# Performance work log

Measured on AMD Instinct MI355X. Metric: run time of the kernel, lower is better.

## Reference

```python
import jax, jax.numpy as jnp
import numpy as np

N_NODES = 100000
N_EDGES = 1600000
D_IN, D_HID, D_OUT = 128, 64, 64


def setup_inputs() -> dict:
    key = jax.random.key(0)
    k0, k1, k2, k3 = jax.random.split(key, 4)
    X = jax.random.normal(k0, (N_NODES, D_IN), dtype=jnp.float32)
    E = jax.random.randint(k1, (2, N_EDGES), 0, N_NODES, dtype=jnp.int32)
    W1 = jax.random.normal(k2, (D_IN, D_HID), dtype=jnp.float32) * 0.05
    b1 = jnp.zeros((D_HID,), dtype=jnp.float32)
    W2 = jax.random.normal(k3, (D_HID, D_OUT), dtype=jnp.float32) * 0.05
    b2 = jnp.zeros((D_OUT,), dtype=jnp.float32)
    return {"V": N_NODES, "E": E, "X": X, "W1": W1, "b1": b1, "W2": W2, "b2": b2}


def _gcn_layer(X, W, b, src, dst, norm, n):
    # GCNConv: linear transform (no bias), gather, degree-normalize, scatter-add, + bias
    Xl = X @ W                              # [n, d_out]
    msg = Xl[src] * norm[:, None]           # [n_edges_sl, d_out] gather
    out = jax.ops.segment_sum(msg, dst, num_segments=n)  # scatter-add
    return out + b


def reference(V, E, X, W1, b1, W2, b2):
    n = X.shape[0]
    # add self loops (add_self_loops=True)
    loop = jnp.arange(n, dtype=E.dtype)
    src = jnp.concatenate([E[0], loop])
    dst = jnp.concatenate([E[1], loop])
    # symmetric gcn_norm: deg over target nodes (unit edge weights)
    deg = jax.ops.segment_sum(jnp.ones_like(dst, dtype=X.dtype), dst, num_segments=n)
    dinv = jnp.where(deg > 0, jax.lax.rsqrt(deg), 0.0)
    norm = dinv[src] * dinv[dst]
    H = jax.nn.relu(_gcn_layer(X, W1, b1, src, dst, norm, n))
    # last layer: no ReLU (matches torch module)
    return _gcn_layer(H, W2, b2, src, dst, norm, n)
```

## Files before the change

### kernel.cpp

```cpp
#include <hip/hip_runtime.h>

#define NT 256
#define NG 512
#define NB 1024
#define TILE 256
#define TILE_SH 8
#define BSTRIDE 8192
#define BSTRIDE_SH 13
#define EPB 4096
#define ITB 16
#define NBUCK_PAD 512

static inline int cdiv(long long a, long long b) { return (int)((a + b - 1) / b); }

typedef unsigned int uint32;
typedef unsigned short ushort16;
typedef short bf16x8 __attribute__((ext_vector_type(8)));
typedef float f32x4 __attribute__((ext_vector_type(4)));

__device__ __forceinline__ ushort16 f2bf(float f) {
  uint32 u = __float_as_uint(f);
  u = (u + 0x7FFF + ((u >> 16) & 1)) >> 16;
  return (ushort16)u;
}
__device__ __forceinline__ float bflo(uint32 w) { return __uint_as_float(w << 16); }
__device__ __forceinline__ float bfhi(uint32 w) { return __uint_as_float(w & 0xFFFF0000u); }
__device__ __forceinline__ float bf2f(ushort16 h) { return __uint_as_float(((uint32)h) << 16); }

template <int K, int NTH>
__device__ __forceinline__ void stage_W(const float* __restrict__ W,
                                        unsigned short* __restrict__ Wt) {
  constexpr int STR = K + 8;
  for (int i = threadIdx.x; i < K * 64; i += NTH) {
    int k = i >> 6, nn = i & 63;
    Wt[nn * STR + k] = f2bf(W[i]);
  }
}

template <int K, int SPLIT>
__device__ __forceinline__ void gemm_tile(const void* __restrict__ Xp,
                                          const unsigned short* __restrict__ Wt,
                                          uint2* __restrict__ Yb, int n, int base) {
  constexpr int STR = K + 8;
  const int tid = threadIdx.x;
  const int w = tid >> 6;
  const int lane = tid & 63;
  const int r = lane & 15;
  const int quad = lane >> 4;
  const int rloc = w * 16 + r;
  const int v = base + rloc;

  f32x4 acc[4];
#pragma unroll
  for (int i = 0; i < 4; ++i) acc[i] = (f32x4)(0.f);

  const float4* X4 = (const float4*)Xp;
  float4 a[K / 32][2];
#pragma unroll
  for (int ks = 0; ks < K / 32; ++ks) {
    a[ks][0] = make_float4(0.f, 0.f, 0.f, 0.f);
    a[ks][1] = make_float4(0.f, 0.f, 0.f, 0.f);
    if (v < n) {
      a[ks][0] = X4[(size_t)v * (K / 4) + ks * 8 + quad * 2];
      a[ks][1] = X4[(size_t)v * (K / 4) + ks * 8 + quad * 2 + 1];
    }
  }
#pragma unroll
  for (int ks = 0; ks < K / 32; ++ks) {
    float f[8] = {a[ks][0].x, a[ks][0].y, a[ks][0].z, a[ks][0].w,
                  a[ks][1].x, a[ks][1].y, a[ks][1].z, a[ks][1].w};
    bf16x8 xh, xl;
#pragma unroll
    for (int j = 0; j < 8; ++j) {
      ushort16 h = f2bf(f[j]);
      xh[j] = (short)h;
      if (SPLIT) xl[j] = (short)f2bf(f[j] - bf2f(h));
    }
    const int koff = ks * 32 + quad * 8;
#pragma unroll
    for (int nt = 0; nt < 4; ++nt) {
      bf16x8 wf = *(const bf16x8*)&Wt[(nt * 16 + r) * STR + koff];
      if (SPLIT)
        acc[nt] = __builtin_amdgcn_mfma_f32_16x16x32_bf16(wf, xl, acc[nt], 0, 0, 0);
      acc[nt] = __builtin_amdgcn_mfma_f32_16x16x32_bf16(wf, xh, acc[nt], 0, 0, 0);
    }
  }

  if (v < n) {
#pragma unroll
    for (int nt = 0; nt < 4; ++nt) {
      uint2 u;
      u.x = (uint32)f2bf(acc[nt][0]) | ((uint32)f2bf(acc[nt][1]) << 16);
      u.y = (uint32)f2bf(acc[nt][2]) | ((uint32)f2bf(acc[nt][3]) << 16);
      Yb[(size_t)v * 16 + nt * 4 + quad] = u;
    }
  }
}

template <int K>
__device__ __forceinline__ void gemm_tile_lds8(const unsigned short* __restrict__ Hs,
                                               const unsigned short* __restrict__ Wt,
                                               uint2* __restrict__ Yb, int n,
                                               int base) {
  constexpr int STR = K + 8;
  const int tid = threadIdx.x;
  const int w = tid >> 6;
  const int wr = w & 3;
  const int nh = w >> 2;
  const int lane = tid & 63;
  const int r = lane & 15;
  const int quad = lane >> 4;
  const int rloc = wr * 16 + r;
  const int v = base + rloc;

  f32x4 acc[2];
#pragma unroll
  for (int i = 0; i < 2; ++i) acc[i] = (f32x4)(0.f);
#pragma unroll
  for (int ks = 0; ks < K / 32; ++ks) {
    const int koff = ks * 32 + quad * 8;
    bf16x8 xf = *(const bf16x8*)&Hs[rloc * STR + koff];
#pragma unroll
    for (int i = 0; i < 2; ++i) {
      const int nt = nh * 2 + i;
      bf16x8 wf = *(const bf16x8*)&Wt[(nt * 16 + r) * STR + koff];
      acc[i] = __builtin_amdgcn_mfma_f32_16x16x32_bf16(wf, xf, acc[i], 0, 0, 0);
    }
  }
  if (v < n) {
#pragma unroll
    for (int i = 0; i < 2; ++i) {
      const int nt = nh * 2 + i;
      uint2 u;
      u.x = (uint32)f2bf(acc[i][0]) | ((uint32)f2bf(acc[i][1]) << 16);
      u.y = (uint32)f2bf(acc[i][2]) | ((uint32)f2bf(acc[i][3]) << 16);
      Yb[(size_t)v * 16 + nt * 4 + quad] = u;
    }
  }
}

struct ScatSh {
  int cnt[NBUCK_PAD];
  int lcur[NBUCK_PAD];
  int delta[NBUCK_PAD];
  int hs[NT];
  uint32 sorted[EPB];
  unsigned short bid[EPB];
};
union FusedSh {
  unsigned short wt[64 * 136];
  ScatSh s;
};

__global__ __launch_bounds__(NT, 4) void k_fused(
    const int* __restrict__ src, const int* __restrict__ dst,
    int* __restrict__ bcursor, int* __restrict__ tileCtr,
    uint32* __restrict__ buck, int nE, int nbuck, int gscat, int ntile,
    const float* __restrict__ X, const float* __restrict__ W1,
    uint2* __restrict__ Yb, int n) {
  __shared__ FusedSh sm;
  __shared__ int stile;
  const int t = threadIdx.x;
  if ((int)blockIdx.x < gscat) {
    for (int i = t; i < NBUCK_PAD; i += NT) sm.s.cnt[i] = 0;
    __syncthreads();
    const int e0 = blockIdx.x * EPB;
    const int ne = min(EPB, nE - e0);
    int dreg[ITB];
#pragma unroll
    for (int it = 0; it < ITB; ++it) {
      int e = e0 + it * NT + t;
      dreg[it] = (e < nE) ? dst[e] : -1;
      if (dreg[it] >= 0) atomicAdd(&sm.s.cnt[dreg[it] >> TILE_SH], 1);
    }
    __syncthreads();
    int c0 = sm.s.cnt[2 * t], c1 = sm.s.cnt[2 * t + 1];
    int ps = c0 + c1;
    sm.s.hs[t] = ps;
    __syncthreads();
    for (int o = 1; o < NT; o <<= 1) {
      int x = (t >= o) ? sm.s.hs[t - o] : 0;
      __syncthreads();
      sm.s.hs[t] += x;
      __syncthreads();
    }
    int lb0 = sm.s.hs[t] - ps;
    int lb1 = lb0 + c0;
    sm.s.lcur[2 * t] = lb0;
    sm.s.lcur[2 * t + 1] = lb1;
    {
      int b0 = 2 * t, b1 = 2 * t + 1;
      if (b0 < nbuck) {
        int g0 = c0 ? atomicAdd(&bcursor[b0], c0) : 0;
        sm.s.delta[b0] = (b0 << BSTRIDE_SH) + g0 - lb0;
      }
      if (b1 < nbuck) {
        int g1 = c1 ? atomicAdd(&bcursor[b1], c1) : 0;
        sm.s.delta[b1] = (b1 << BSTRIDE_SH) + g1 - lb1;
      }
    }
    __syncthreads();
#pragma unroll
    for (int it = 0; it < ITB; ++it) {
      int e = e0 + it * NT + t;
      if (dreg[it] >= 0) {
        int d = dreg[it];
        int b = d >> TILE_SH;
        int p = atomicAdd(&sm.s.lcur[b], 1);
        sm.s.sorted[p] = (uint32)src[e] | ((uint32)(d & (TILE - 1)) << 24);
        sm.s.bid[p] = (unsigned short)b;
      }
    }
    __syncthreads();
    for (int i = t; i < ne; i += NT) {
      int b = sm.s.bid[i];
      int g = sm.s.delta[b] + i;
      if (g < ((b + 1) << BSTRIDE_SH))
        buck[g] = sm.s.sorted[i];
    }
    __syncthreads();
  }
  stage_W<128, NT>(W1, sm.wt);
  __syncthreads();
  for (;;) {
    if (t == 0) stile = atomicAdd(tileCtr, 1);
    __syncthreads();
    int tile = stile;
    __syncthreads();
    if (tile >= ntile) break;
    gemm_tile<128, 1>(X, sm.wt, Yb, n, tile * 64);
  }
}

__global__ __launch_bounds__(NB) void k_bcsr(const uint32* __restrict__ buck,
                                             const int* __restrict__ bcursor,
                                             int2* __restrict__ rowspan,
                                             float* __restrict__ dinv,
                                             int* __restrict__ srcs, int n) {
  __shared__ int hist[TILE];
  __shared__ int hs[TILE];
  __shared__ int off[TILE];
  __shared__ uint32 sarr[BSTRIDE];
  const int b = blockIdx.x;
  const int t = threadIdx.x;
  const int W = b * BSTRIDE;
  const int cntb = min(bcursor[b], BSTRIDE);
  const int v0 = b << TILE_SH;
  const int nv = min(TILE, n - v0);
  if (t < TILE) hist[t] = 0;
  __syncthreads();
  for (int i = t; i < cntb; i += NB) atomicAdd(&hist[buck[W + i] >> 24], 1);
  __syncthreads();
  int h = (t < TILE) ? hist[t] : 0;
  if (t < TILE) hs[t] = h;
  __syncthreads();
  for (int o = 1; o < TILE; o <<= 1) {
    int x = (t >= o && t < TILE) ? hs[t - o] : 0;
    __syncthreads();
    if (t < TILE) hs[t] += x;
    __syncthreads();
  }
  if (t < TILE) {
    int ex = hs[t] - h;
    off[t] = ex;
    if (t < nv) {
      rowspan[v0 + t] = make_int2(W + ex, W + ex + h);
      dinv[v0 + t] = rsqrtf((float)(h + 1));
    }
  }
  __syncthreads();
  for (int i = t; i < cntb; i += NB) {
    uint32 w = buck[W + i];
    int ld = (int)(w >> 24);
    int p = atomicAdd(&off[ld], 1);
    sarr[p] = w & 0x00FFFFFFu;
  }
  __syncthreads();
  for (int i = t; i < cntb; i += NB) srcs[W + i] = (int)sarr[i];
}

struct Acc8 {
  float a0, a1, a2, a3, a4, a5, a6, a7;
  __device__ __forceinline__ void madd(uint4 r, float s) {
    a0 = fmaf(bflo(r.x), s, a0); a1 = fmaf(bfhi(r.x), s, a1);
    a2 = fmaf(bflo(r.y), s, a2); a3 = fmaf(bfhi(r.y), s, a3);
    a4 = fmaf(bflo(r.z), s, a4); a5 = fmaf(bfhi(r.z), s, a5);
    a6 = fmaf(bflo(r.w), s, a6); a7 = fmaf(bfhi(r.w), s, a7);
  }
};

__device__ __forceinline__ void agg_node(const int* __restrict__ srcs,
                                         const float* __restrict__ dinv,
                                         const uint4* __restrict__ Y, int beg,
                                         int end, int part, int q, Acc8& A) {
  int j = beg + q;
  for (; j + 12 < end; j += 16) {
    int s0 = srcs[j];
    int s1 = srcs[j + 4];
    int s2 = srcs[j + 8];
    int s3 = srcs[j + 12];
    float d0 = dinv[s0], d1 = dinv[s1], d2 = dinv[s2], d3 = dinv[s3];
    uint4 r0 = Y[(size_t)s0 * 8 + part];
    uint4 r1 = Y[(size_t)s1 * 8 + part];
    uint4 r2 = Y[(size_t)s2 * 8 + part];
    uint4 r3 = Y[(size_t)s3 * 8 + part];
    A.madd(r0, d0);
    A.madd(r1, d1);
    A.madd(r2, d2);
    A.madd(r3, d3);
  }
  if (j + 4 < end) {
    int s0 = srcs[j];
    int s1 = srcs[j + 4];
    float d0 = dinv[s0], d1 = dinv[s1];
    uint4 r0 = Y[(size_t)s0 * 8 + part];
    uint4 r1 = Y[(size_t)s1 * 8 + part];
    A.madd(r0, d0);
    A.madd(r1, d1);
    j += 8;
  }
  if (j < end) {
    int s = srcs[j];
    A.madd(Y[(size_t)s * 8 + part], dinv[s]);
  }
}

#define L1STR 72

__global__ __launch_bounds__(NG, 4) void k_gather_l1(
    const int2* __restrict__ rowspan, const int* __restrict__ srcs,
    const float* __restrict__ dinv, const uint4* __restrict__ Y1,
    const float* __restrict__ bias, const float* __restrict__ W2,
    uint2* __restrict__ Y2, int n) {
  __shared__ unsigned short Wt[64 * L1STR];
  __shared__ unsigned short Hs[64 * L1STR];
  stage_W<64, NG>(W2, Wt);

  const int tid = threadIdx.x;
  const int lane = tid & 63;
  const int l5 = lane & 31;
  const int part = l5 & 7;
  const int q = l5 >> 3;
  const int grp = ((tid >> 6) << 1) + (lane >> 5);
  const int base = blockIdx.x * 64;

#pragma unroll 1
  for (int p = 0; p < 4; ++p) {
    const int local = p * 16 + grp;
    const int v = base + local;
    const bool act = v < n;
    int2 rs = act ? rowspan[v] : make_int2(0, 0);
    const float dv = act ? dinv[v] : 0.f;
    uint4 wv = act ? Y1[(size_t)v * 8 + part] : make_uint4(0u, 0u, 0u, 0u);
    Acc8 A = {0.f, 0.f, 0.f, 0.f, 0.f, 0.f, 0.f, 0.f};
    agg_node(srcs, dinv, Y1, rs.x, rs.y, part, q, A);
#pragma unroll
    for (int m = 8; m <= 16; m <<= 1) {
      A.a0 += __shfl_xor(A.a0, m);
      A.a1 += __shfl_xor(A.a1, m);
      A.a2 += __shfl_xor(A.a2, m);
      A.a3 += __shfl_xor(A.a3, m);
      A.a4 += __shfl_xor(A.a4, m);
      A.a5 += __shfl_xor(A.a5, m);
      A.a6 += __shfl_xor(A.a6, m);
      A.a7 += __shfl_xor(A.a7, m);
    }
    if (q == 0 && act) {
      const float4* b4 = (const float4*)bias;
      float4 b0 = b4[part * 2], b1 = b4[part * 2 + 1];
      float r0 = fmaxf(dv * (A.a0 + dv * bflo(wv.x)) + b0.x, 0.f);
      float r1 = fmaxf(dv * (A.a1 + dv * bfhi(wv.x)) + b0.y, 0.f);
      float r2 = fmaxf(dv * (A.a2 + dv * bflo(wv.y)) + b0.z, 0.f);
      float r3 = fmaxf(dv * (A.a3 + dv * bfhi(wv.y)) + b0.w, 0.f);
      float r4 = fmaxf(dv * (A.a4 + dv * bflo(wv.z)) + b1.x, 0.f);
      float r5 = fmaxf(dv * (A.a5 + dv * bfhi(wv.z)) + b1.y, 0.f);
      float r6 = fmaxf(dv * (A.a6 + dv * bflo(wv.w)) + b1.z, 0.f);
      float r7 = fmaxf(dv * (A.a7 + dv * bfhi(wv.w)) + b1.w, 0.f);
      uint4 u;
      u.x = (uint32)f2bf(r0) | ((uint32)f2bf(r1) << 16);
      u.y = (uint32)f2bf(r2) | ((uint32)f2bf(r3) << 16);
      u.z = (uint32)f2bf(r4) | ((uint32)f2bf(r5) << 16);
      u.w = (uint32)f2bf(r6) | ((uint32)f2bf(r7) << 16);
      *(uint4*)&Hs[local * L1STR + part * 8] = u;
    }
  }
  __syncthreads();
  gemm_tile_lds8<64>(Hs, Wt, Y2, n, base);
}

__global__ __launch_bounds__(NT) void k_gather2(const int2* __restrict__ rowspan,
                                                const int* __restrict__ srcs,
                                                const float* __restrict__ dinv,
                                                const uint4* __restrict__ Xn,
                                                const float* __restrict__ bias,
                                                float* __restrict__ outp, int n) {
  const int gt = blockIdx.x * NT + threadIdx.x;
  const int lane = threadIdx.x & 63;
  const int v = ((gt >> 6) << 1) + (lane >> 5);
  if (v >= n) return;
  const int l5 = lane & 31;
  const int part = l5 & 7;
  const int q = l5 >> 3;
  const int2 rs = rowspan[v];
  const float dv = dinv[v];
  uint4 wv = Xn[(size_t)v * 8 + part];
  Acc8 A = {0.f, 0.f, 0.f, 0.f, 0.f, 0.f, 0.f, 0.f};
  agg_node(srcs, dinv, Xn, rs.x, rs.y, part, q, A);
#pragma unroll
  for (int m = 8; m <= 16; m <<= 1) {
    A.a0 += __shfl_xor(A.a0, m);
    A.a1 += __shfl_xor(A.a1, m);
    A.a2 += __shfl_xor(A.a2, m);
    A.a3 += __shfl_xor(A.a3, m);
    A.a4 += __shfl_xor(A.a4, m);
    A.a5 += __shfl_xor(A.a5, m);
    A.a6 += __shfl_xor(A.a6, m);
    A.a7 += __shfl_xor(A.a7, m);
  }
  if (q == 0) {
    const float4* b4 = (const float4*)bias;
    float4 b0 = b4[part * 2], b1 = b4[part * 2 + 1];
    float r0 = dv * (A.a0 + dv * bflo(wv.x)) + b0.x;
    float r1 = dv * (A.a1 + dv * bfhi(wv.x)) + b0.y;
    float r2 = dv * (A.a2 + dv * bflo(wv.y)) + b0.z;
    float r3 = dv * (A.a3 + dv * bfhi(wv.y)) + b0.w;
    float r4 = dv * (A.a4 + dv * bflo(wv.z)) + b1.x;
    float r5 = dv * (A.a5 + dv * bfhi(wv.z)) + b1.y;
    float r6 = dv * (A.a6 + dv * bflo(wv.w)) + b1.z;
    float r7 = dv * (A.a7 + dv * bfhi(wv.w)) + b1.w;
    float4* o4 = (float4*)outp;
    o4[(size_t)v * 16 + part * 2] = make_float4(r0, r1, r2, r3);
    o4[(size_t)v * 16 + part * 2 + 1] = make_float4(r4, r5, r6, r7);
  }
}

extern "C" void kernel_launch(void* const* d_in, const int* in_sizes, int n_in,
                              void* d_out, int out_size, void* d_ws, size_t ws_size,
                              hipStream_t stream) {
  const int* E = (const int*)d_in[1];
  const float* X = (const float*)d_in[2];
  const float* W1 = (const float*)d_in[3];
  const float* b1 = (const float*)d_in[4];
  const float* W2 = (const float*)d_in[5];
  const float* b2 = (const float*)d_in[6];
  float* out = (float*)d_out;

  const int n = in_sizes[2] / 128;
  const int nE = in_sizes[1] / 2;
  const int* src = E;
  const int* dst = E + nE;
  const int nbuck = cdiv(n, TILE);

  char* ws = (char*)d_ws;
  size_t off = 0;
  auto alloc = [&](size_t bytes) {
    size_t o = off;
    off = (off + bytes + 255) & ~(size_t)255;
    return (void*)(ws + o);
  };
  int2* rowspan = (int2*)alloc((size_t)n * 8);
  float* dinv = (float*)alloc((size_t)n * 4);
  int* bcursor = (int*)alloc((size_t)(nbuck + 1) * 4);
  int* tileCtr = bcursor + nbuck;
  uint32* buck = (uint32*)alloc((size_t)nbuck * BSTRIDE * 4);
  int* srcs = (int*)alloc((size_t)nbuck * BSTRIDE * 4);
  uint2* Y1 = (uint2*)alloc((size_t)n * 64 * 2);
  uint2* Y2 = (uint2*)alloc((size_t)n * 64 * 2);

  const int gscat = cdiv(nE, EPB);
  const int ntile = cdiv(n, 64);
  const int gfused = 1024;
  const int gthreads_blocks = cdiv((long long)n * 32, NT);

  hipMemsetAsync(bcursor, 0, (size_t)(nbuck + 1) * 4, stream);

  k_fused<<<gfused, NT, 0, stream>>>(src, dst, bcursor, tileCtr, buck, nE,
                                     nbuck, gscat, ntile, X, W1, Y1, n);
  k_bcsr<<<nbuck, NB, 0, stream>>>(buck, bcursor, rowspan, dinv, srcs, n);

  k_gather_l1<<<ntile, NG, 0, stream>>>(rowspan, srcs, dinv, (const uint4*)Y1,
                                        b1, W2, Y2, n);

  k_gather2<<<gthreads_blocks, NT, 0, stream>>>(rowspan, srcs, dinv,
                                                (const uint4*)Y2, b2, out, n);
}
```

Before: 239.7 us.

## Split layer-1 GEMM tiles between scatter and bucket-CSR kernels for overlap

Splits the dense X@W1 tile work into two parts. The first SPLIT tiles run in the scatter-fused kernel and the rest run in the bucket-CSR kernel, which now also stages W1 and pulls tiles from a second counter after building CSR rows. Tiles are claimed four at a time to reduce atomic traffic. The scatter chunk size is halved and grid and occupancy bounds are raised so more blocks share the scatter phase. The intent is to hide the latency-bound sort phases behind GEMM work, at the cost of a fixed split constant tuned for this graph size and a larger grid in the second kernel.

```diff
diff --git a/kernel.cpp b/kernel.cpp
--- a/kernel.cpp
+++ b/kernel.cpp
@@ -7,9 +7,10 @@
 #define TILE_SH 8
 #define BSTRIDE 8192
 #define BSTRIDE_SH 13
-#define EPB 4096
-#define ITB 16
+#define EPB 2048
+#define ITB 8
 #define NBUCK_PAD 512
+#define SPLIT 768
 
 static inline int cdiv(long long a, long long b) { return (int)((a + b - 1) / b); }
 
@@ -37,12 +38,12 @@
   }
 }
 
-template <int K, int SPLIT>
+template <int K, int SPLITLO>
 __device__ __forceinline__ void gemm_tile(const void* __restrict__ Xp,
                                           const unsigned short* __restrict__ Wt,
-                                          uint2* __restrict__ Yb, int n, int base) {
+                                          uint2* __restrict__ Yb, int n, int base,
+                                          int tid) {
   constexpr int STR = K + 8;
-  const int tid = threadIdx.x;
   const int w = tid >> 6;
   const int lane = tid & 63;
   const int r = lane & 15;
@@ -74,13 +75,13 @@
     for (int j = 0; j < 8; ++j) {
       ushort16 h = f2bf(f[j]);
       xh[j] = (short)h;
-      if (SPLIT) xl[j] = (short)f2bf(f[j] - bf2f(h));
+      if (SPLITLO) xl[j] = (short)f2bf(f[j] - bf2f(h));
     }
     const int koff = ks * 32 + quad * 8;
 #pragma unroll
     for (int nt = 0; nt < 4; ++nt) {
       bf16x8 wf = *(const bf16x8*)&Wt[(nt * 16 + r) * STR + koff];
-      if (SPLIT)
+      if (SPLITLO)
         acc[nt] = __builtin_amdgcn_mfma_f32_16x16x32_bf16(wf, xl, acc[nt], 0, 0, 0);
       acc[nt] = __builtin_amdgcn_mfma_f32_16x16x32_bf16(wf, xh, acc[nt], 0, 0, 0);
     }
@@ -152,10 +153,10 @@
   ScatSh s;
 };
 
-__global__ __launch_bounds__(NT, 4) void k_fused(
+__global__ __launch_bounds__(NT, 6) void k_fused(
     const int* __restrict__ src, const int* __restrict__ dst,
     int* __restrict__ bcursor, int* __restrict__ tileCtr,
-    uint32* __restrict__ buck, int nE, int nbuck, int gscat, int ntile,
+    uint32* __restrict__ buck, int nE, int nbuck, int gscat, int split,
     const float* __restrict__ X, const float* __restrict__ W1,
     uint2* __restrict__ Yb, int n) {
   __shared__ FusedSh sm;
@@ -223,60 +224,89 @@
   stage_W<128, NT>(W1, sm.wt);
   __syncthreads();
   for (;;) {
-    if (t == 0) stile = atomicAdd(tileCtr, 1);
-    __syncthreads();
-    int tile = stile;
-    __syncthreads();
-    if (tile >= ntile) break;
-    gemm_tile<128, 1>(X, sm.wt, Yb, n, tile * 64);
-  }
-}
-
-__global__ __launch_bounds__(NB) void k_bcsr(const uint32* __restrict__ buck,
-                                             const int* __restrict__ bcursor,
-                                             int2* __restrict__ rowspan,
-                                             float* __restrict__ dinv,
-                                             int* __restrict__ srcs, int n) {
-  __shared__ int hist[TILE];
-  __shared__ int hs[TILE];
-  __shared__ int off[TILE];
-  __shared__ uint32 sarr[BSTRIDE];
+    if (t == 0) stile = atomicAdd(tileCtr, 4);
+    __syncthreads();
+    const int base = stile;
+    __syncthreads();
+    if (base >= split) break;
+#pragma unroll 1
+    for (int c = 0; c < 4; ++c) {
+      int tile = base + c;
+      if (tile < split) gemm_tile<128, 1>(X, sm.wt, Yb, n, tile * 64, t);
+    }
+  }
+}
+
+union BcsrSh {
+  struct {
+    int hist[TILE];
+    int hs[TILE];
+    int off[TILE];
+    uint32 sarr[BSTRIDE];
+  } c;
+  unsigned short wt[64 * 136];
+};
+
+__global__ __launch_bounds__(NB, 8) void k_bcsr_gemm(
+    const uint32* __restrict__ buck, const int* __restrict__ bcursor,
+    int2* __restrict__ rowspan, float* __restrict__ dinv,
+    int* __restrict__ srcs, int n, int nbuck, const float* __restrict__ X,
+    const float* __restrict__ W1, uint2* __restrict__ Yb,
+    int* __restrict__ tileCtr2, int split, int ntile) {
+  __shared__ BcsrSh sm;
+  __shared__ int stile;
+  const int t = threadIdx.x;
   const int b = blockIdx.x;
-  const int t = threadIdx.x;
-  const int W = b * BSTRIDE;
-  const int cntb = min(bcursor[b], BSTRIDE);
-  const int v0 = b << TILE_SH;
-  const int nv = min(TILE, n - v0);
-  if (t < TILE) hist[t] = 0;
+  if (b < nbuck) {
+    const int W = b * BSTRIDE;
+    const int cntb = min(bcursor[b], BSTRIDE);
+    const int v0 = b << TILE_SH;
+    const int nv = min(TILE, n - v0);
+    if (t < TILE) sm.c.hist[t] = 0;
+    __syncthreads();
+    for (int i = t; i < cntb; i += NB) atomicAdd(&sm.c.hist[buck[W + i] >> 24], 1);
+    __syncthreads();
+    int h = (t < TILE) ? sm.c.hist[t] : 0;
+    if (t < TILE) sm.c.hs[t] = h;
+    __syncthreads();
+    for (int o = 1; o < TILE; o <<= 1) {
+      int x = (t >= o && t < TILE) ? sm.c.hs[t - o] : 0;
+      __syncthreads();
+      if (t < TILE) sm.c.hs[t] += x;
+      __syncthreads();
+    }
+    if (t < TILE) {
+      int ex = sm.c.hs[t] - h;
+      sm.c.off[t] = ex;
+      if (t < nv) {
+        rowspan[v0 + t] = make_int2(W + ex, W + ex + h);
+        dinv[v0 + t] = rsqrtf((float)(h + 1));
+      }
+    }
+    __syncthreads();
+    for (int i = t; i < cntb; i += NB) {
+      uint32 w = buck[W + i];
+      int ld = (int)(w >> 24);
+      int p = atomicAdd(&sm.c.off[ld], 1);
+      sm.c.sarr[p] = w & 0x00FFFFFFu;
+    }
+    __syncthreads();
+    for (int i = t; i < cntb; i += NB) srcs[W + i] = (int)sm.c.sarr[i];
+    __syncthreads();
+  }
+  stage_W<128, NB>(W1, sm.wt);
   __syncthreads();
-  for (int i = t; i < cntb; i += NB) atomicAdd(&hist[buck[W + i] >> 24], 1);
-  __syncthreads();
-  int h = (t < TILE) ? hist[t] : 0;
-  if (t < TILE) hs[t] = h;
-  __syncthreads();
-  for (int o = 1; o < TILE; o <<= 1) {
-    int x = (t >= o && t < TILE) ? hs[t - o] : 0;
-    __syncthreads();
-    if (t < TILE) hs[t] += x;
-    __syncthreads();
-  }
-  if (t < TILE) {
-    int ex = hs[t] - h;
-    off[t] = ex;
-    if (t < nv) {
-      rowspan[v0 + t] = make_int2(W + ex, W + ex + h);
-      dinv[v0 + t] = rsqrtf((float)(h + 1));
-    }
-  }
-  __syncthreads();
-  for (int i = t; i < cntb; i += NB) {
-    uint32 w = buck[W + i];
-    int ld = (int)(w >> 24);
-    int p = atomicAdd(&off[ld], 1);
-    sarr[p] = w & 0x00FFFFFFu;
-  }
-  __syncthreads();
-  for (int i = t; i < cntb; i += NB) srcs[W + i] = (int)sarr[i];
+  const int g = t >> 8;
+  const int lt = t & 255;
+  for (;;) {
+    if (t == 0) stile = atomicAdd(tileCtr2, 4);
+    __syncthreads();
+    const int base = split + stile;
+    __syncthreads();
+    if (base >= ntile) break;
+    const int tile = base + g;
+    if (tile < ntile) gemm_tile<128, 1>(X, sm.wt, Yb, n, tile * 64, lt);
+  }
 }
 
 struct Acc8 {
@@ -460,8 +490,9 @@
   };
   int2* rowspan = (int2*)alloc((size_t)n * 8);
   float* dinv = (float*)alloc((size_t)n * 4);
-  int* bcursor = (int*)alloc((size_t)(nbuck + 1) * 4);
+  int* bcursor = (int*)alloc((size_t)(nbuck + 2) * 4);
   int* tileCtr = bcursor + nbuck;
+  int* tileCtr2 = bcursor + nbuck + 1;
   uint32* buck = (uint32*)alloc((size_t)nbuck * BSTRIDE * 4);
   int* srcs = (int*)alloc((size_t)nbuck * BSTRIDE * 4);
   uint2* Y1 = (uint2*)alloc((size_t)n * 64 * 2);
@@ -469,14 +500,15 @@
 
   const int gscat = cdiv(nE, EPB);
   const int ntile = cdiv(n, 64);
-  const int gfused = 1024;
+  const int gfused = 1536;
   const int gthreads_blocks = cdiv((long long)n * 32, NT);
 
-  hipMemsetAsync(bcursor, 0, (size_t)(nbuck + 1) * 4, stream);
+  hipMemsetAsync(bcursor, 0, (size_t)(nbuck + 2) * 4, stream);
 
   k_fused<<<gfused, NT, 0, stream>>>(src, dst, bcursor, tileCtr, buck, nE,
-                                     nbuck, gscat, ntile, X, W1, Y1, n);
-  k_bcsr<<<nbuck, NB, 0, stream>>>(buck, bcursor, rowspan, dinv, srcs, n);
+                                     nbuck, gscat, SPLIT, X, W1, Y1, n);
+  k_bcsr_gemm<<<1024, NB, 0, stream>>>(buck, bcursor, rowspan, dinv, srcs, n,
+                                       nbuck, X, W1, Y1, tileCtr2, SPLIT, ntile);
 
   k_gather_l1<<<ntile, NG, 0, stream>>>(rowspan, srcs, dinv, (const uint4*)Y1,
                                         b1, W2, Y2, n);
```

After: 257.7 us. 1.07x slower.

## Use 512-thread fused blocks with static GEMM tile split instead of atomic tile counter

Applied to the files above, without the earlier changes.

Doubles the fused scatter/GEMM kernel block size to 512 threads, which halves per-thread edge iterations and turns the bucket scan into one bucket per thread. The dynamic atomic tile counter is replaced by a static assignment: non-scatter blocks take the first T0 tiles and scatter blocks take the rest in a strided loop, with tiles now covering 128 rows across 8 waves. This removes the per-tile global atomic and its two barriers. The static split may unbalance work, because scatter blocks start their GEMM tiles late, and occupancy changes with the larger blocks.

```diff
diff --git a/kernel.cpp b/kernel.cpp
--- a/kernel.cpp
+++ b/kernel.cpp
@@ -1,6 +1,7 @@
 #include <hip/hip_runtime.h>
 
 #define NT 256
+#define NF 512
 #define NG 512
 #define NB 1024
 #define TILE 256
@@ -8,8 +9,9 @@
 #define BSTRIDE 8192
 #define BSTRIDE_SH 13
 #define EPB 4096
-#define ITB 16
+#define ITB 8
 #define NBUCK_PAD 512
+#define GTILE 128
 
 static inline int cdiv(long long a, long long b) { return (int)((a + b - 1) / b); }
 
@@ -37,18 +39,17 @@
   }
 }
 
-template <int K, int SPLIT>
-__device__ __forceinline__ void gemm_tile(const void* __restrict__ Xp,
-                                          const unsigned short* __restrict__ Wt,
-                                          uint2* __restrict__ Yb, int n, int base) {
+template <int K>
+__device__ __forceinline__ void gemm_tile8(const float* __restrict__ Xp,
+                                           const unsigned short* __restrict__ Wt,
+                                           uint2* __restrict__ Yb, int n, int base) {
   constexpr int STR = K + 8;
   const int tid = threadIdx.x;
   const int w = tid >> 6;
   const int lane = tid & 63;
   const int r = lane & 15;
   const int quad = lane >> 4;
-  const int rloc = w * 16 + r;
-  const int v = base + rloc;
+  const int v = base + w * 16 + r;
 
   f32x4 acc[4];
 #pragma unroll
@@ -74,14 +75,13 @@
     for (int j = 0; j < 8; ++j) {
       ushort16 h = f2bf(f[j]);
       xh[j] = (short)h;
-      if (SPLIT) xl[j] = (short)f2bf(f[j] - bf2f(h));
+      xl[j] = (short)f2bf(f[j] - bf2f(h));
     }
     const int koff = ks * 32 + quad * 8;
 #pragma unroll
     for (int nt = 0; nt < 4; ++nt) {
       bf16x8 wf = *(const bf16x8*)&Wt[(nt * 16 + r) * STR + koff];
-      if (SPLIT)
-        acc[nt] = __builtin_amdgcn_mfma_f32_16x16x32_bf16(wf, xl, acc[nt], 0, 0, 0);
+      acc[nt] = __builtin_amdgcn_mfma_f32_16x16x32_bf16(wf, xl, acc[nt], 0, 0, 0);
       acc[nt] = __builtin_amdgcn_mfma_f32_16x16x32_bf16(wf, xh, acc[nt], 0, 0, 0);
     }
   }
@@ -143,7 +143,7 @@
   int cnt[NBUCK_PAD];
   int lcur[NBUCK_PAD];
   int delta[NBUCK_PAD];
-  int hs[NT];
+  int hs[NF];
   uint32 sorted[EPB];
   unsigned short bid[EPB];
 };
@@ -152,57 +152,46 @@
   ScatSh s;
 };
 
-__global__ __launch_bounds__(NT, 4) void k_fused(
+__global__ __launch_bounds__(NF) void k_fused(
     const int* __restrict__ src, const int* __restrict__ dst,
-    int* __restrict__ bcursor, int* __restrict__ tileCtr,
-    uint32* __restrict__ buck, int nE, int nbuck, int gscat, int ntile,
-    const float* __restrict__ X, const float* __restrict__ W1,
-    uint2* __restrict__ Yb, int n) {
+    int* __restrict__ bcursor, uint32* __restrict__ buck, int nE, int nbuck,
+    int gscat, int t0, int ntile, const float* __restrict__ X,
+    const float* __restrict__ W1, uint2* __restrict__ Yb, int n) {
   __shared__ FusedSh sm;
-  __shared__ int stile;
   const int t = threadIdx.x;
-  if ((int)blockIdx.x < gscat) {
-    for (int i = t; i < NBUCK_PAD; i += NT) sm.s.cnt[i] = 0;
+  const bool isScat = (int)blockIdx.x < gscat;
+  if (isScat) {
+    sm.s.cnt[t] = 0;
     __syncthreads();
     const int e0 = blockIdx.x * EPB;
     const int ne = min(EPB, nE - e0);
     int dreg[ITB];
 #pragma unroll
     for (int it = 0; it < ITB; ++it) {
-      int e = e0 + it * NT + t;
+      int e = e0 + it * NF + t;
       dreg[it] = (e < nE) ? dst[e] : -1;
       if (dreg[it] >= 0) atomicAdd(&sm.s.cnt[dreg[it] >> TILE_SH], 1);
     }
     __syncthreads();
-    int c0 = sm.s.cnt[2 * t], c1 = sm.s.cnt[2 * t + 1];
-    int ps = c0 + c1;
-    sm.s.hs[t] = ps;
-    __syncthreads();
-    for (int o = 1; o < NT; o <<= 1) {
+    int c = sm.s.cnt[t];
+    sm.s.hs[t] = c;
+    __syncthreads();
+    for (int o = 1; o < NF; o <<= 1) {
       int x = (t >= o) ? sm.s.hs[t - o] : 0;
       __syncthreads();
       sm.s.hs[t] += x;
       __syncthreads();
     }
-    int lb0 = sm.s.hs[t] - ps;
-    int lb1 = lb0 + c0;
-    sm.s.lcur[2 * t] = lb0;
-    sm.s.lcur[2 * t + 1] = lb1;
-    {
-      int b0 = 2 * t, b1 = 2 * t + 1;
-      if (b0 < nbuck) {
-        int g0 = c0 ? atomicAdd(&bcursor[b0], c0) : 0;
-        sm.s.delta[b0] = (b0 << BSTRIDE_SH) + g0 - lb0;
-      }
-      if (b1 < nbuck) {
-        int g1 = c1 ? atomicAdd(&bcursor[b1], c1) : 0;
-        sm.s.delta[b1] = (b1 << BSTRIDE_SH) + g1 - lb1;
-      }
+    int lb = sm.s.hs[t] - c;
+    sm.s.lcur[t] = lb;
+    if (t < nbuck) {
+      int g = c ? atomicAdd(&bcursor[t], c) : 0;
+      sm.s.delta[t] = (t << BSTRIDE_SH) + g - lb;
     }
     __syncthreads();
 #pragma unroll
     for (int it = 0; it < ITB; ++it) {
-      int e = e0 + it * NT + t;
+      int e = e0 + it * NF + t;
       if (dreg[it] >= 0) {
         int d = dreg[it];
         int b = d >> TILE_SH;
@@ -212,7 +201,7 @@
       }
     }
     __syncthreads();
-    for (int i = t; i < ne; i += NT) {
+    for (int i = t; i < ne; i += NF) {
       int b = sm.s.bid[i];
       int g = sm.s.delta[b] + i;
       if (g < ((b + 1) << BSTRIDE_SH))
@@ -220,15 +209,15 @@
     }
     __syncthreads();
   }
-  stage_W<128, NT>(W1, sm.wt);
-  __syncthreads();
-  for (;;) {
-    if (t == 0) stile = atomicAdd(tileCtr, 1);
-    __syncthreads();
-    int tile = stile;
-    __syncthreads();
-    if (tile >= ntile) break;
-    gemm_tile<128, 1>(X, sm.wt, Yb, n, tile * 64);
+  stage_W<128, NF>(W1, sm.wt);
+  __syncthreads();
+  if (isScat) {
+    for (int tile = t0 + (int)blockIdx.x; tile < ntile; tile += gscat)
+      gemm_tile8<128>(X, sm.wt, Yb, n, tile * GTILE);
+  } else {
+    const int gg = gridDim.x - gscat;
+    for (int tile = (int)blockIdx.x - gscat; tile < t0; tile += gg)
+      gemm_tile8<128>(X, sm.wt, Yb, n, tile * GTILE);
   }
 }
 
@@ -460,26 +449,28 @@
   };
   int2* rowspan = (int2*)alloc((size_t)n * 8);
   float* dinv = (float*)alloc((size_t)n * 4);
-  int* bcursor = (int*)alloc((size_t)(nbuck + 1) * 4);
-  int* tileCtr = bcursor + nbuck;
+  int* bcursor = (int*)alloc((size_t)nbuck * 4);
   uint32* buck = (uint32*)alloc((size_t)nbuck * BSTRIDE * 4);
   int* srcs = (int*)alloc((size_t)nbuck * BSTRIDE * 4);
   uint2* Y1 = (uint2*)alloc((size_t)n * 64 * 2);
   uint2* Y2 = (uint2*)alloc((size_t)n * 64 * 2);
 
   const int gscat = cdiv(nE, EPB);
-  const int ntile = cdiv(n, 64);
+  const int ntile = cdiv(n, GTILE);
   const int gfused = 1024;
+  const int ggemm = gfused - gscat;
+  const int T0 = ggemm;
+  const int ntile64 = cdiv(n, 64);
   const int gthreads_blocks = cdiv((long long)n * 32, NT);
 
-  hipMemsetAsync(bcursor, 0, (size_t)(nbuck + 1) * 4, stream);
-
-  k_fused<<<gfused, NT, 0, stream>>>(src, dst, bcursor, tileCtr, buck, nE,
-                                     nbuck, gscat, ntile, X, W1, Y1, n);
+  hipMemsetAsync(bcursor, 0, (size_t)nbuck * 4, stream);
+
+  k_fused<<<gfused, NF, 0, stream>>>(src, dst, bcursor, buck, nE, nbuck, gscat,
+                                     T0, ntile, X, W1, Y1, n);
   k_bcsr<<<nbuck, NB, 0, stream>>>(buck, bcursor, rowspan, dinv, srcs, n);
 
-  k_gather_l1<<<ntile, NG, 0, stream>>>(rowspan, srcs, dinv, (const uint4*)Y1,
-                                        b1, W2, Y2, n);
+  k_gather_l1<<<ntile64, NG, 0, stream>>>(rowspan, srcs, dinv, (const uint4*)Y1,
+                                          b1, W2, Y2, n);
 
   k_gather2<<<gthreads_blocks, NT, 0, stream>>>(rowspan, srcs, dinv,
                                                 (const uint4*)Y2, b2, out, n);
```

After: 224.7 us. 1.07x faster.
